# Optimization experiments

Measured on AMD Instinct MI355X. Metric: run time of the kernel, lower is better.

The kernel has to match this reference:

```python
import jax, jax.numpy as jnp
import numpy as np

B, S, D, H = 4, 2048, 1024, 16
HD = D // H  # head_dim = 64


def setup_inputs() -> dict:
    key = jax.random.key(0)
    k1, k2, k3 = jax.random.split(key, 3)
    scale = 0.02
    return {
        "hidden_states": jax.random.normal(k1, (B, S, D), dtype=jnp.float32),
        "W_attn": jax.random.normal(k2, (D, 3 * D), dtype=jnp.float32) * scale,
        "b_attn": jnp.zeros((3 * D,), dtype=jnp.float32),
        "W_proj": jax.random.normal(k3, (D, D), dtype=jnp.float32) * scale,
        "b_proj": jnp.zeros((D,), dtype=jnp.float32),
    }


def reference(hidden_states, W_attn, b_attn, W_proj, b_proj):
    b, s, d = hidden_states.shape
    qkv = hidden_states @ W_attn + b_attn  # [B,S,3D]
    q, k, v = jnp.split(qkv, 3, axis=-1)
    # [B,S,D] -> [B,H,S,hd]
    def to_heads(x):
        return x.reshape(b, s, H, HD).transpose(0, 2, 1, 3)
    q, k, v = to_heads(q), to_heads(k), to_heads(v)
    scores = jnp.einsum("bhqd,bhkd->bhqk", q, k) / jnp.sqrt(jnp.float32(HD))
    causal = jnp.tril(jnp.ones((s, s), dtype=bool))  # [S,S]
    scores = jnp.where(causal[None, None], scores, jnp.float32(-jnp.inf))
    probs = jax.nn.softmax(scores, axis=-1)  # dropout p=0 -> identity (eval)
    out = jnp.einsum("bhqk,bhkd->bhqd", probs, v)  # [B,H,S,hd]
    out = out.transpose(0, 2, 1, 3).reshape(b, s, d)
    return out @ W_proj + b_proj
```

## Files before the change

### kernel.cpp

```cpp
#include <hip/hip_runtime.h>
#include <hip/hip_bf16.h>


typedef float f32x4 __attribute__((ext_vector_type(4)));
typedef __bf16 bf16x8 __attribute__((ext_vector_type(8)));
typedef unsigned short u16x8 __attribute__((ext_vector_type(8)));
typedef unsigned short u16x4 __attribute__((ext_vector_type(4)));

static constexpr int Sq = 2048, Dm = 1024, HD = 64, N3 = 3072;
static constexpr int Mrows = 4 * Sq;
static constexpr float SM_SCALE = 0.18033688011112042f;
static constexpr float SM_BIAS  = -11.541560327111707f;

__device__ __forceinline__ unsigned short f2bf(float f) {
  return __builtin_bit_cast(unsigned short, (__bf16)f);
}
__device__ __forceinline__ f32x4 mfma16(u16x8 a, u16x8 b, f32x4 c) {
  return __builtin_amdgcn_mfma_f32_16x16x32_bf16(
      __builtin_bit_cast(bf16x8, a), __builtin_bit_cast(bf16x8, b), c, 0, 0, 0);
}

__global__ __launch_bounds__(256) void cvt_k(
    const float* __restrict__ in, unsigned short* __restrict__ out, int n) {
  int stride = gridDim.x * 256 * 4;
  for (int i = (blockIdx.x * 256 + threadIdx.x) * 4; i < n; i += stride) {
    f32x4 v = *reinterpret_cast<const f32x4*>(&in[i]);
    u16x4 o;
    #pragma unroll
    for (int j = 0; j < 4; j++) o[j] = f2bf(v[j]);
    *reinterpret_cast<u16x4*>(&out[i]) = o;
  }
}

__global__ __launch_bounds__(256) void tcvt_k(
    const float* __restrict__ in, unsigned short* __restrict__ out,
    int R, int C) {
  __shared__ float tile[32][33];
  int c0 = blockIdx.x * 32, r0 = blockIdx.y * 32;
  int tx = threadIdx.x & 31, ty = threadIdx.x >> 5;
  #pragma unroll
  for (int i = 0; i < 32; i += 8)
    tile[ty + i][tx] = in[(size_t)(r0 + ty + i) * C + c0 + tx];
  __syncthreads();
  #pragma unroll
  for (int i = 0; i < 32; i += 8)
    out[(size_t)(c0 + ty + i) * R + r0 + tx] = f2bf(tile[tx][ty + i]);
}

template <bool OUT_F32>
__global__ __launch_bounds__(256) void gemm_bt(
    const unsigned short* __restrict__ A, const unsigned short* __restrict__ Bt,
    const float* __restrict__ bias, void* __restrict__ Cout,
    int Md, int Nd, int Kd) {
  __shared__ unsigned short Asm[128 * 32];
  __shared__ unsigned short Bsm[128 * 32];
  int t = threadIdx.x;
  int wave = t >> 6, lane = t & 63;
  int lrow = lane & 15, lq = lane >> 4;
  int wr = wave >> 1, wc = wave & 1;
  int bm = blockIdx.y * 128, bn = blockIdx.x * 128;
  f32x4 acc[4][4] = {};

  for (int k0 = 0; k0 < Kd; k0 += 32) {
    __syncthreads();
    #pragma unroll
    for (int c = 0; c < 2; c++) {
      int e = c * 2048 + t * 8;
      int row = e >> 5, col = e & 31;
      const unsigned short* ga = A + (size_t)(bm + row) * Kd + k0 + col;
      const unsigned short* gb = Bt + (size_t)(bn + row) * Kd + k0 + col;
      __builtin_amdgcn_global_load_lds(
          (const __attribute__((address_space(1))) void*)ga,
          (__attribute__((address_space(3))) void*)((char*)Asm + c * 4096 + wave * 1024),
          16, 0, 0);
      __builtin_amdgcn_global_load_lds(
          (const __attribute__((address_space(1))) void*)gb,
          (__attribute__((address_space(3))) void*)((char*)Bsm + c * 4096 + wave * 1024),
          16, 0, 0);
    }
    __syncthreads();

    u16x8 af[4], bfr[4];
    #pragma unroll
    for (int m = 0; m < 4; m++)
      af[m] = *reinterpret_cast<const u16x8*>(&Asm[(wr * 64 + m * 16 + lrow) * 32 + lq * 8]);
    #pragma unroll
    for (int n = 0; n < 4; n++)
      bfr[n] = *reinterpret_cast<const u16x8*>(&Bsm[(wc * 64 + n * 16 + lrow) * 32 + lq * 8]);
    #pragma unroll
    for (int m = 0; m < 4; m++)
      #pragma unroll
      for (int n = 0; n < 4; n++)
        acc[m][n] = mfma16(af[m], bfr[n], acc[m][n]);
  }

  #pragma unroll
  for (int n = 0; n < 4; n++) {
    int col = bn + wc * 64 + n * 16 + lrow;
    float bv = bias[col];
    #pragma unroll
    for (int m = 0; m < 4; m++) {
      #pragma unroll
      for (int j = 0; j < 4; j++) {
        int row = bm + wr * 64 + m * 16 + lq * 4 + j;
        if constexpr (OUT_F32)
          ((float*)Cout)[(size_t)row * Nd + col] = acc[m][n][j] + bv;
        else
          ((unsigned short*)Cout)[(size_t)row * Nd + col] = f2bf(acc[m][n][j] + bv);
      }
    }
  }
}

__global__ __launch_bounds__(256) void attn_k(
    const unsigned short* __restrict__ qkv,
    unsigned short* __restrict__ ao) {
  int bh = blockIdx.y;
  int b = bh >> 4, h = bh & 15;
  int t = threadIdx.x, wave = t >> 6, lane = t & 63;
  int lrow = lane & 15, lq = lane >> 4;

  __shared__ unsigned short Kl[2][64][72];
  __shared__ unsigned short Vt[2][64][72];
  __shared__ unsigned short Pl[4][16][72];

  const size_t base = (size_t)b * Sq * N3;
  const unsigned short* Kbase = qkv + base + Dm + h * HD;
  const unsigned short* Vbase = qkv + base + 2 * Dm + h * HD;

  int irow = t >> 2, icol = (t & 3) * 16;
  int vd = lane, vkb = wave;

  u16x8 kr0, kr1, vr0, vr1;
  auto prefetch = [&](int kv) {
    const unsigned short* kp = Kbase + (size_t)(kv + irow) * N3 + icol;
    kr0 = *reinterpret_cast<const u16x8*>(kp);
    kr1 = *reinterpret_cast<const u16x8*>(kp + 8);
    const unsigned short* vp = Vbase + (size_t)kv * N3 + vd;
    #pragma unroll
    for (int i = 0; i < 8; i++) {
      vr0[i] = vp[(size_t)(vkb * 8 + i) * N3];
      vr1[i] = vp[(size_t)(32 + vkb * 8 + i) * N3];
    }
  };

  #pragma unroll 1
  for (int pass = 0; pass < 2; ++pass) {
    int qb = pass ? (int)blockIdx.x : 15 - (int)blockIdx.x;
    int q0 = qb * 128;
    int ntiles = 2 * qb + 2;

    u16x8 qf[2][2];
    #pragma unroll
    for (int m = 0; m < 2; m++) {
      const unsigned short* qp =
          qkv + base + (size_t)(q0 + wave * 32 + m * 16 + lrow) * N3 + h * HD + lq * 8;
      qf[m][0] = *reinterpret_cast<const u16x8*>(qp);
      qf[m][1] = *reinterpret_cast<const u16x8*>(qp + 32);
    }

    float lrun[2] = {0.f, 0.f};
    f32x4 oacc[2][4] = {};

    prefetch(0);

    #pragma unroll 1
    for (int kt = 0; kt < ntiles; ++kt) {
      int kv = kt * 64, bsel = kt & 1;
      *reinterpret_cast<u16x8*>(&Kl[bsel][irow][icol]) = kr0;
      *reinterpret_cast<u16x8*>(&Kl[bsel][irow][icol + 8]) = kr1;
      *reinterpret_cast<u16x8*>(&Vt[bsel][vd][vkb * 8]) = vr0;
      *reinterpret_cast<u16x8*>(&Vt[bsel][vd][32 + vkb * 8]) = vr1;
      if (kt + 1 < ntiles) prefetch(kv + 64);
      __syncthreads();

      u16x8 kf0[4], kf1[4], vf0[4], vf1[4];
      #pragma unroll
      for (int ct = 0; ct < 4; ct++) {
        kf0[ct] = *reinterpret_cast<const u16x8*>(&Kl[bsel][ct * 16 + lrow][lq * 8]);
        kf1[ct] = *reinterpret_cast<const u16x8*>(&Kl[bsel][ct * 16 + lrow][32 + lq * 8]);
      }
      f32x4 sacc[2][4] = {};
      #pragma unroll
      for (int m = 0; m < 2; m++)
        #pragma unroll
        for (int ct = 0; ct < 4; ct++) {
          sacc[m][ct] = mfma16(kf0[ct], qf[m][0], sacc[m][ct]);
          sacc[m][ct] = mfma16(kf1[ct], qf[m][1], sacc[m][ct]);
        }
      #pragma unroll
      for (int ht = 0; ht < 4; ht++) {
        vf0[ht] = *reinterpret_cast<const u16x8*>(&Vt[bsel][ht * 16 + lrow][lq * 8]);
        vf1[ht] = *reinterpret_cast<const u16x8*>(&Vt[bsel][ht * 16 + lrow][32 + lq * 8]);
      }

      #pragma unroll
      for (int m = 0; m < 2; m++) {
        int rwm = q0 + wave * 32 + m * 16;
        bool need_mask = kv + 63 > rwm;
        int dlim = rwm - kv + lrow;
        float p[4][4];
        #pragma unroll
        for (int ct = 0; ct < 4; ct++) {
          #pragma unroll
          for (int j = 0; j < 4; j++) {
            float e = exp2f(fmaf(sacc[m][ct][j], SM_SCALE, SM_BIAS));
            if (need_mask) e = (16 * ct + 4 * lq + j <= dlim) ? e : 0.f;
            p[ct][j] = e;
            lrun[m] += e;
          }
        }

        #pragma unroll
        for (int ct = 0; ct < 4; ct++) {
          u16x4 o;
          #pragma unroll
          for (int j = 0; j < 4; j++) o[j] = f2bf(p[ct][j]);
          *reinterpret_cast<u16x4*>(&Pl[wave][lrow][16 * ct + 4 * lq]) = o;
        }

        u16x8 pa0 = *reinterpret_cast<const u16x8*>(&Pl[wave][lrow][lq * 8]);
        u16x8 pa1 = *reinterpret_cast<const u16x8*>(&Pl[wave][lrow][32 + lq * 8]);
        #pragma unroll
        for (int ht = 0; ht < 4; ht++) {
          oacc[m][ht] = mfma16(pa0, vf0[ht], oacc[m][ht]);
          oacc[m][ht] = mfma16(pa1, vf1[ht], oacc[m][ht]);
        }
      }
    }

    #pragma unroll
    for (int m = 0; m < 2; m++) {
      float r = lrun[m];
      r += __shfl_xor(r, 16);
      r += __shfl_xor(r, 32);
      lrun[m] = r;
    }

    #pragma unroll
    for (int m = 0; m < 2; m++) {
      float inv[4];
      #pragma unroll
      for (int j = 0; j < 4; j++)
        inv[j] = __builtin_amdgcn_rcpf(__shfl(lrun[m], lq * 4 + j));
      #pragma unroll
      for (int ht = 0; ht < 4; ht++)
        #pragma unroll
        for (int j = 0; j < 4; j++) {
          int rg = q0 + wave * 32 + m * 16 + lq * 4 + j;
          float v = oacc[m][ht][j] * inv[j];
          ao[(size_t)(b * Sq + rg) * Dm + h * HD + ht * 16 + lrow] = f2bf(v);
        }
    }
  }
}

extern "C" void kernel_launch(void* const* d_in, const int* in_sizes, int n_in,
                              void* d_out, int out_size, void* d_ws, size_t ws_size,
                              hipStream_t stream) {
  const float* hs = (const float*)d_in[0];
  const float* Wa = (const float*)d_in[1];
  const float* ba = (const float*)d_in[2];
  const float* Wp = (const float*)d_in[3];
  const float* bp = (const float*)d_in[4];
  float* out = (float*)d_out;

  char* ws = (char*)d_ws;
  unsigned short* QKV = (unsigned short*)ws;
  unsigned short* WaT = (unsigned short*)(ws + 50331648);
  unsigned short* AO  = (unsigned short*)(ws + 50331648);
  unsigned short* WpT = (unsigned short*)ws;
  unsigned short* hsB = (unsigned short*)d_out;

  cvt_k<<<2048, 256, 0, stream>>>(hs, hsB, Mrows * Dm);
  tcvt_k<<<dim3(96, 32), 256, 0, stream>>>(Wa, WaT, 1024, 3072);
  gemm_bt<false><<<dim3(24, 64), 256, 0, stream>>>(hsB, WaT, ba, QKV, Mrows, N3, Dm);
  attn_k<<<dim3(8, 64), 256, 0, stream>>>(QKV, AO);
  tcvt_k<<<dim3(32, 32), 256, 0, stream>>>(Wp, WpT, 1024, 1024);
  gemm_bt<true><<<dim3(8, 64), 256, 0, stream>>>(AO, WpT, bp, out, Mrows, Dm, Dm);
}
```

Baseline: 212.9 us.

## Shrink attention query tile to 64 rows and compute row sums via MFMA

Each attention block now handles 64-row query tiles (one 16-row strip per wave) instead of 128, and the grid doubles to 1024 blocks. The softmax scale is folded into Q and the bias into the score accumulator init, and the row-sum is computed with an MFMA against a ones vector instead of scalar adds plus shuffles. The first tile of the second pass is prefetched while the first pass finishes, with the double-buffer selector carried across passes. This is meant to improve occupancy and load balance and to cut VALU work. The cost is that K/V tiles are reused across half as many query rows, which adds K/V loads, and rounding the scaled Q to bf16 adds a little error.

```diff
diff --git a/kernel.cpp b/kernel.cpp
--- a/kernel.cpp
+++ b/kernel.cpp
@@ -12,6 +12,9 @@
 static constexpr float SM_SCALE = 0.18033688011112042f;
 static constexpr float SM_BIAS  = -11.541560327111707f;
 
+__device__ __forceinline__ float bf2f(unsigned short u) {
+  union { unsigned u32; float f; } x; x.u32 = ((unsigned)u) << 16; return x.f;
+}
 __device__ __forceinline__ unsigned short f2bf(float f) {
   return __builtin_bit_cast(unsigned short, (__bf16)f);
 }
@@ -131,6 +134,10 @@
   int irow = t >> 2, icol = (t & 3) * 16;
   int vd = lane, vkb = wave;
 
+  u16x8 ones;
+  #pragma unroll
+  for (int j = 0; j < 8; j++) ones[j] = 0x3F80;
+
   u16x8 kr0, kr1, vr0, vr1;
   auto prefetch = [&](int kv) {
     const unsigned short* kp = Kbase + (size_t)(kv + irow) * N3 + icol;
@@ -144,114 +151,95 @@
     }
   };
 
+  int bsel = 0;
+
   #pragma unroll 1
   for (int pass = 0; pass < 2; ++pass) {
-    int qb = pass ? (int)blockIdx.x : 15 - (int)blockIdx.x;
-    int q0 = qb * 128;
-    int ntiles = 2 * qb + 2;
-
-    u16x8 qf[2][2];
-    #pragma unroll
-    for (int m = 0; m < 2; m++) {
+    int qb = pass ? (int)blockIdx.x : 31 - (int)blockIdx.x;
+    int q0 = qb * 64;
+    int ntiles = qb + 1;
+    int rwm = q0 + wave * 16;
+
+    u16x8 qf0, qf1;
+    {
       const unsigned short* qp =
-          qkv + base + (size_t)(q0 + wave * 32 + m * 16 + lrow) * N3 + h * HD + lq * 8;
-      qf[m][0] = *reinterpret_cast<const u16x8*>(qp);
-      qf[m][1] = *reinterpret_cast<const u16x8*>(qp + 32);
-    }
-
-    float lrun[2] = {0.f, 0.f};
-    f32x4 oacc[2][4] = {};
-
-    prefetch(0);
+          qkv + base + (size_t)(rwm + lrow) * N3 + h * HD + lq * 8;
+      u16x8 r0 = *reinterpret_cast<const u16x8*>(qp);
+      u16x8 r1 = *reinterpret_cast<const u16x8*>(qp + 32);
+      #pragma unroll
+      for (int j = 0; j < 8; j++) {
+        qf0[j] = f2bf(SM_SCALE * bf2f(r0[j]));
+        qf1[j] = f2bf(SM_SCALE * bf2f(r1[j]));
+      }
+    }
+
+    f32x4 oacc[4] = {};
+    f32x4 dacc = {};
+
+    if (pass == 0) prefetch(0);
 
     #pragma unroll 1
     for (int kt = 0; kt < ntiles; ++kt) {
-      int kv = kt * 64, bsel = kt & 1;
+      int kv = kt * 64;
       *reinterpret_cast<u16x8*>(&Kl[bsel][irow][icol]) = kr0;
       *reinterpret_cast<u16x8*>(&Kl[bsel][irow][icol + 8]) = kr1;
       *reinterpret_cast<u16x8*>(&Vt[bsel][vd][vkb * 8]) = vr0;
       *reinterpret_cast<u16x8*>(&Vt[bsel][vd][32 + vkb * 8]) = vr1;
       if (kt + 1 < ntiles) prefetch(kv + 64);
+      else if (pass == 0) prefetch(0);
       __syncthreads();
 
-      u16x8 kf0[4], kf1[4], vf0[4], vf1[4];
+      f32x4 sacc[4];
+      #pragma unroll
+      for (int ct = 0; ct < 4; ct++)
+        sacc[ct] = f32x4{SM_BIAS, SM_BIAS, SM_BIAS, SM_BIAS};
       #pragma unroll
       for (int ct = 0; ct < 4; ct++) {
-        kf0[ct] = *reinterpret_cast<const u16x8*>(&Kl[bsel][ct * 16 + lrow][lq * 8]);
-        kf1[ct] = *reinterpret_cast<const u16x8*>(&Kl[bsel][ct * 16 + lrow][32 + lq * 8]);
-      }
-      f32x4 sacc[2][4] = {};
-      #pragma unroll
-      for (int m = 0; m < 2; m++)
-        #pragma unroll
-        for (int ct = 0; ct < 4; ct++) {
-          sacc[m][ct] = mfma16(kf0[ct], qf[m][0], sacc[m][ct]);
-          sacc[m][ct] = mfma16(kf1[ct], qf[m][1], sacc[m][ct]);
-        }
-      #pragma unroll
-      for (int ht = 0; ht < 4; ht++) {
-        vf0[ht] = *reinterpret_cast<const u16x8*>(&Vt[bsel][ht * 16 + lrow][lq * 8]);
-        vf1[ht] = *reinterpret_cast<const u16x8*>(&Vt[bsel][ht * 16 + lrow][32 + lq * 8]);
-      }
-
-      #pragma unroll
-      for (int m = 0; m < 2; m++) {
-        int rwm = q0 + wave * 32 + m * 16;
-        bool need_mask = kv + 63 > rwm;
-        int dlim = rwm - kv + lrow;
-        float p[4][4];
-        #pragma unroll
-        for (int ct = 0; ct < 4; ct++) {
-          #pragma unroll
-          for (int j = 0; j < 4; j++) {
-            float e = exp2f(fmaf(sacc[m][ct][j], SM_SCALE, SM_BIAS));
-            if (need_mask) e = (16 * ct + 4 * lq + j <= dlim) ? e : 0.f;
-            p[ct][j] = e;
-            lrun[m] += e;
-          }
-        }
-
-        #pragma unroll
-        for (int ct = 0; ct < 4; ct++) {
-          u16x4 o;
-          #pragma unroll
-          for (int j = 0; j < 4; j++) o[j] = f2bf(p[ct][j]);
-          *reinterpret_cast<u16x4*>(&Pl[wave][lrow][16 * ct + 4 * lq]) = o;
-        }
-
-        u16x8 pa0 = *reinterpret_cast<const u16x8*>(&Pl[wave][lrow][lq * 8]);
-        u16x8 pa1 = *reinterpret_cast<const u16x8*>(&Pl[wave][lrow][32 + lq * 8]);
-        #pragma unroll
-        for (int ht = 0; ht < 4; ht++) {
-          oacc[m][ht] = mfma16(pa0, vf0[ht], oacc[m][ht]);
-          oacc[m][ht] = mfma16(pa1, vf1[ht], oacc[m][ht]);
-        }
-      }
-    }
-
-    #pragma unroll
-    for (int m = 0; m < 2; m++) {
-      float r = lrun[m];
-      r += __shfl_xor(r, 16);
-      r += __shfl_xor(r, 32);
-      lrun[m] = r;
-    }
-
-    #pragma unroll
-    for (int m = 0; m < 2; m++) {
-      float inv[4];
-      #pragma unroll
-      for (int j = 0; j < 4; j++)
-        inv[j] = __builtin_amdgcn_rcpf(__shfl(lrun[m], lq * 4 + j));
-      #pragma unroll
-      for (int ht = 0; ht < 4; ht++)
+        u16x8 kf0 = *reinterpret_cast<const u16x8*>(&Kl[bsel][ct * 16 + lrow][lq * 8]);
+        u16x8 kf1 = *reinterpret_cast<const u16x8*>(&Kl[bsel][ct * 16 + lrow][32 + lq * 8]);
+        sacc[ct] = mfma16(kf0, qf0, sacc[ct]);
+        sacc[ct] = mfma16(kf1, qf1, sacc[ct]);
+      }
+
+      bool need_mask = kv + 63 > rwm;
+      int dlim = rwm - kv + lrow;
+      #pragma unroll
+      for (int ct = 0; ct < 4; ct++) {
+        u16x4 o;
         #pragma unroll
         for (int j = 0; j < 4; j++) {
-          int rg = q0 + wave * 32 + m * 16 + lq * 4 + j;
-          float v = oacc[m][ht][j] * inv[j];
-          ao[(size_t)(b * Sq + rg) * Dm + h * HD + ht * 16 + lrow] = f2bf(v);
+          float e = exp2f(sacc[ct][j]);
+          if (need_mask) e = (16 * ct + 4 * lq + j <= dlim) ? e : 0.f;
+          o[j] = f2bf(e);
         }
-    }
+        *reinterpret_cast<u16x4*>(&Pl[wave][lrow][16 * ct + 4 * lq]) = o;
+      }
+
+      u16x8 pa0 = *reinterpret_cast<const u16x8*>(&Pl[wave][lrow][lq * 8]);
+      u16x8 pa1 = *reinterpret_cast<const u16x8*>(&Pl[wave][lrow][32 + lq * 8]);
+      dacc = mfma16(pa0, ones, dacc);
+      dacc = mfma16(pa1, ones, dacc);
+      #pragma unroll
+      for (int ht = 0; ht < 4; ht++) {
+        u16x8 vf0 = *reinterpret_cast<const u16x8*>(&Vt[bsel][ht * 16 + lrow][lq * 8]);
+        u16x8 vf1 = *reinterpret_cast<const u16x8*>(&Vt[bsel][ht * 16 + lrow][32 + lq * 8]);
+        oacc[ht] = mfma16(pa0, vf0, oacc[ht]);
+        oacc[ht] = mfma16(pa1, vf1, oacc[ht]);
+      }
+      bsel ^= 1;
+    }
+
+    float inv[4];
+    #pragma unroll
+    for (int j = 0; j < 4; j++) inv[j] = __builtin_amdgcn_rcpf(dacc[j]);
+    #pragma unroll
+    for (int ht = 0; ht < 4; ht++)
+      #pragma unroll
+      for (int j = 0; j < 4; j++) {
+        int rg = rwm + lq * 4 + j;
+        float v = oacc[ht][j] * inv[j];
+        ao[(size_t)(b * Sq + rg) * Dm + h * HD + ht * 16 + lrow] = f2bf(v);
+      }
   }
 }
 
@@ -275,7 +263,7 @@
   cvt_k<<<2048, 256, 0, stream>>>(hs, hsB, Mrows * Dm);
   tcvt_k<<<dim3(96, 32), 256, 0, stream>>>(Wa, WaT, 1024, 3072);
   gemm_bt<false><<<dim3(24, 64), 256, 0, stream>>>(hsB, WaT, ba, QKV, Mrows, N3, Dm);
-  attn_k<<<dim3(8, 64), 256, 0, stream>>>(QKV, AO);
+  attn_k<<<dim3(16, 64), 256, 0, stream>>>(QKV, AO);
   tcvt_k<<<dim3(32, 32), 256, 0, stream>>>(Wp, WpT, 1024, 1024);
   gemm_bt<true><<<dim3(8, 64), 256, 0, stream>>>(AO, WpT, bp, out, Mrows, Dm, Dm);
 }
```

After: 228.7 us. 7.4% more time.

## Fold softmax scale into Q, compute row sums via MFMA, prefetch across passes

Applied to the files above, without the earlier changes.

Pre-scales Q by the softmax scale and initialises score accumulators with the bias, so the exp needs no per-element FMA. Row sums are accumulated with an extra MFMA against a ones vector instead of scalar adds and cross-lane shuffles. The first K/V tile of the second pass is prefetched during the last tile of the first pass, and MFMA sections are wrapped in s_setprio. Rounding Q to bf16 after scaling slightly changes numerics, and the row sum now adds up bf16-rounded probabilities.

```diff
diff --git a/kernel.cpp b/kernel.cpp
--- a/kernel.cpp
+++ b/kernel.cpp
@@ -12,6 +12,9 @@
 static constexpr float SM_SCALE = 0.18033688011112042f;
 static constexpr float SM_BIAS  = -11.541560327111707f;
 
+__device__ __forceinline__ float bf2f(unsigned short u) {
+  union { unsigned u32; float f; } x; x.u32 = ((unsigned)u) << 16; return x.f;
+}
 __device__ __forceinline__ unsigned short f2bf(float f) {
   return __builtin_bit_cast(unsigned short, (__bf16)f);
 }
@@ -131,6 +134,10 @@
   int irow = t >> 2, icol = (t & 3) * 16;
   int vd = lane, vkb = wave;
 
+  u16x8 ones;
+  #pragma unroll
+  for (int j = 0; j < 8; j++) ones[j] = 0x3F80;
+
   u16x8 kr0, kr1, vr0, vr1;
   auto prefetch = [&](int kv) {
     const unsigned short* kp = Kbase + (size_t)(kv + irow) * N3 + icol;
@@ -149,20 +156,26 @@
     int qb = pass ? (int)blockIdx.x : 15 - (int)blockIdx.x;
     int q0 = qb * 128;
     int ntiles = 2 * qb + 2;
+    int rw0 = q0 + wave * 32;
 
     u16x8 qf[2][2];
     #pragma unroll
     for (int m = 0; m < 2; m++) {
       const unsigned short* qp =
-          qkv + base + (size_t)(q0 + wave * 32 + m * 16 + lrow) * N3 + h * HD + lq * 8;
-      qf[m][0] = *reinterpret_cast<const u16x8*>(qp);
-      qf[m][1] = *reinterpret_cast<const u16x8*>(qp + 32);
-    }
-
-    float lrun[2] = {0.f, 0.f};
+          qkv + base + (size_t)(rw0 + m * 16 + lrow) * N3 + h * HD + lq * 8;
+      u16x8 r0 = *reinterpret_cast<const u16x8*>(qp);
+      u16x8 r1 = *reinterpret_cast<const u16x8*>(qp + 32);
+      #pragma unroll
+      for (int j = 0; j < 8; j++) {
+        qf[m][0][j] = f2bf(SM_SCALE * bf2f(r0[j]));
+        qf[m][1][j] = f2bf(SM_SCALE * bf2f(r1[j]));
+      }
+    }
+
     f32x4 oacc[2][4] = {};
-
-    prefetch(0);
+    f32x4 dacc[2] = {};
+
+    if (pass == 0) prefetch(0);
 
     #pragma unroll 1
     for (int kt = 0; kt < ntiles; ++kt) {
@@ -172,15 +185,22 @@
       *reinterpret_cast<u16x8*>(&Vt[bsel][vd][vkb * 8]) = vr0;
       *reinterpret_cast<u16x8*>(&Vt[bsel][vd][32 + vkb * 8]) = vr1;
       if (kt + 1 < ntiles) prefetch(kv + 64);
+      else if (pass == 0) prefetch(0);
       __syncthreads();
 
-      u16x8 kf0[4], kf1[4], vf0[4], vf1[4];
+      u16x8 kf0[4], kf1[4];
       #pragma unroll
       for (int ct = 0; ct < 4; ct++) {
         kf0[ct] = *reinterpret_cast<const u16x8*>(&Kl[bsel][ct * 16 + lrow][lq * 8]);
         kf1[ct] = *reinterpret_cast<const u16x8*>(&Kl[bsel][ct * 16 + lrow][32 + lq * 8]);
       }
-      f32x4 sacc[2][4] = {};
+      f32x4 sacc[2][4];
+      #pragma unroll
+      for (int m = 0; m < 2; m++)
+        #pragma unroll
+        for (int ct = 0; ct < 4; ct++)
+          sacc[m][ct] = f32x4{SM_BIAS, SM_BIAS, SM_BIAS, SM_BIAS};
+      __builtin_amdgcn_s_setprio(1);
       #pragma unroll
       for (int m = 0; m < 2; m++)
         #pragma unroll
@@ -188,6 +208,9 @@
           sacc[m][ct] = mfma16(kf0[ct], qf[m][0], sacc[m][ct]);
           sacc[m][ct] = mfma16(kf1[ct], qf[m][1], sacc[m][ct]);
         }
+      __builtin_amdgcn_s_setprio(0);
+
+      u16x8 vf0[4], vf1[4];
       #pragma unroll
       for (int ht = 0; ht < 4; ht++) {
         vf0[ht] = *reinterpret_cast<const u16x8*>(&Vt[bsel][ht * 16 + lrow][lq * 8]);
@@ -196,58 +219,45 @@
 
       #pragma unroll
       for (int m = 0; m < 2; m++) {
-        int rwm = q0 + wave * 32 + m * 16;
+        int rwm = rw0 + m * 16;
         bool need_mask = kv + 63 > rwm;
         int dlim = rwm - kv + lrow;
-        float p[4][4];
-        #pragma unroll
-        for (int ct = 0; ct < 4; ct++) {
-          #pragma unroll
-          for (int j = 0; j < 4; j++) {
-            float e = exp2f(fmaf(sacc[m][ct][j], SM_SCALE, SM_BIAS));
-            if (need_mask) e = (16 * ct + 4 * lq + j <= dlim) ? e : 0.f;
-            p[ct][j] = e;
-            lrun[m] += e;
-          }
-        }
-
         #pragma unroll
         for (int ct = 0; ct < 4; ct++) {
           u16x4 o;
           #pragma unroll
-          for (int j = 0; j < 4; j++) o[j] = f2bf(p[ct][j]);
+          for (int j = 0; j < 4; j++) {
+            float e = exp2f(sacc[m][ct][j]);
+            if (need_mask) e = (16 * ct + 4 * lq + j <= dlim) ? e : 0.f;
+            o[j] = f2bf(e);
+          }
           *reinterpret_cast<u16x4*>(&Pl[wave][lrow][16 * ct + 4 * lq]) = o;
         }
 
         u16x8 pa0 = *reinterpret_cast<const u16x8*>(&Pl[wave][lrow][lq * 8]);
         u16x8 pa1 = *reinterpret_cast<const u16x8*>(&Pl[wave][lrow][32 + lq * 8]);
+        __builtin_amdgcn_s_setprio(1);
+        dacc[m] = mfma16(pa0, ones, dacc[m]);
+        dacc[m] = mfma16(pa1, ones, dacc[m]);
         #pragma unroll
         for (int ht = 0; ht < 4; ht++) {
           oacc[m][ht] = mfma16(pa0, vf0[ht], oacc[m][ht]);
           oacc[m][ht] = mfma16(pa1, vf1[ht], oacc[m][ht]);
         }
-      }
-    }
-
-    #pragma unroll
-    for (int m = 0; m < 2; m++) {
-      float r = lrun[m];
-      r += __shfl_xor(r, 16);
-      r += __shfl_xor(r, 32);
-      lrun[m] = r;
+        __builtin_amdgcn_s_setprio(0);
+      }
     }
 
     #pragma unroll
     for (int m = 0; m < 2; m++) {
       float inv[4];
       #pragma unroll
-      for (int j = 0; j < 4; j++)
-        inv[j] = __builtin_amdgcn_rcpf(__shfl(lrun[m], lq * 4 + j));
+      for (int j = 0; j < 4; j++) inv[j] = __builtin_amdgcn_rcpf(dacc[m][j]);
       #pragma unroll
       for (int ht = 0; ht < 4; ht++)
         #pragma unroll
         for (int j = 0; j < 4; j++) {
-          int rg = q0 + wave * 32 + m * 16 + lq * 4 + j;
+          int rg = rw0 + m * 16 + lq * 4 + j;
           float v = oacc[m][ht][j] * inv[j];
           ao[(size_t)(b * Sq + rg) * Dm + h * HD + ht * 16 + lrow] = f2bf(v);
         }
```

After: 211.2 us. About the same (-0.8%).
